# Optimization experiments

Hardware: AMD Instinct MI355X
Metric: run time of the kernel (lower is better)

## Reference

```python
import jax, jax.numpy as jnp
import numpy as np

HEADS = 16
DIM_HEAD = 64
INNER = HEADS * DIM_HEAD  # 1024
QUERY_DIM = 1024
CONTEXT_DIM = 1024
TEXT_LEN = 77
IMG_SCALE = 1.0
SCALE = DIM_HEAD ** -0.5


def setup_inputs() -> dict:
    key = jax.random.key(0)
    ks = jax.random.split(key, 10)
    B, N, Lc = 16, 2048, 333  # 77 text + 256 image tokens
    x = jax.random.normal(ks[0], (B, N, QUERY_DIM), dtype=jnp.float32)
    context = jax.random.normal(ks[1], (B, Lc, CONTEXT_DIM), dtype=jnp.float32)
    def w(k, din, dout):
        return jax.random.normal(k, (din, dout), dtype=jnp.float32) * (din ** -0.5)
    Wq = w(ks[2], QUERY_DIM, INNER)
    Wk = w(ks[3], CONTEXT_DIM, INNER)
    Wv = w(ks[4], CONTEXT_DIM, INNER)
    Wk_ip = w(ks[5], CONTEXT_DIM, INNER)
    Wv_ip = w(ks[6], CONTEXT_DIM, INNER)
    Wo = w(ks[7], INNER, QUERY_DIM)
    bo = jnp.zeros((QUERY_DIM,), dtype=jnp.float32)
    return {"x": x, "context": context, "Wq": Wq, "Wk": Wk, "Wv": Wv,
            "Wk_ip": Wk_ip, "Wv_ip": Wv_ip, "Wo": Wo, "bo": bo}


def _attend(q, k, v):
    # q: [B,N,H,D], k/v: [B,L,H,D]
    sim = jnp.einsum('bihd,bjhd->bhij', q, k) * SCALE
    attn = jax.nn.softmax(sim, axis=-1)
    out = jnp.einsum('bhij,bjhd->bihd', attn, v)
    B, N, H, D = out.shape
    return out.reshape(B, N, H * D)


def reference(x, context, Wq, Wk, Wv, Wk_ip, Wv_ip, Wo, bo):
    B, N, _ = x.shape
    ctx_txt = context[:, :TEXT_LEN, :]
    ctx_img = context[:, TEXT_LEN:, :]
    q = (x @ Wq).reshape(B, N, HEADS, DIM_HEAD)
    k = (ctx_txt @ Wk).reshape(B, TEXT_LEN, HEADS, DIM_HEAD)
    v = (ctx_txt @ Wv).reshape(B, TEXT_LEN, HEADS, DIM_HEAD)
    out = _attend(q, k, v)
    Li = ctx_img.shape[1]
    k_ip = (ctx_img @ Wk_ip).reshape(B, Li, HEADS, DIM_HEAD)
    v_ip = (ctx_img @ Wv_ip).reshape(B, Li, HEADS, DIM_HEAD)
    out_ip = _attend(q, k_ip, v_ip)
    out = out + IMG_SCALE * out_ip
    return out @ Wo + bo
```

## Files before the change

### kernel.cpp

```cpp
#include <hip/hip_runtime.h>
#include <cstdint>
#include <type_traits>

typedef unsigned short u16;
typedef __attribute__((ext_vector_type(8))) short short8;
typedef __attribute__((ext_vector_type(4))) float f32x4;

__device__ __forceinline__ u16 f2bf(float f) {
  unsigned x;
  __builtin_memcpy(&x, &f, 4);
  x = x + 0x7fffu + ((x >> 16) & 1u);
  return (u16)(x >> 16);
}
__device__ __forceinline__ f32x4 mfma16(short8 a, short8 b, f32x4 c) {
  return __builtin_amdgcn_mfma_f32_16x16x32_bf16(a, b, c, 0, 0, 0);
}
__device__ __forceinline__ void async_cp16(const u16* g, const u16* l) {
  __builtin_amdgcn_global_load_lds(
      (const __attribute__((address_space(1))) unsigned int*)(uintptr_t)g,
      (__attribute__((address_space(3))) unsigned int*)(uintptr_t)l, 16, 0, 0);
}

__global__ __launch_bounds__(256)
void cvt_f32_bf16(const float* __restrict__ s, u16* __restrict__ d, long n4) {
  long i = (long)blockIdx.x * 256 + threadIdx.x;
  if (i < n4) {
    float4 f = ((const float4*)s)[i];
    ushort4 o;
    o.x = f2bf(f.x);
    o.y = f2bf(f.y);
    o.z = f2bf(f.z);
    o.w = f2bf(f.w);
    ((ushort4*)d)[i] = o;
  }
}

__global__ __launch_bounds__(256)
void zero16(u16* __restrict__ p, long n8) {
  long i = (long)blockIdx.x * 256 + threadIdx.x;
  if (i < n8) {
    short8 z = {0, 0, 0, 0, 0, 0, 0, 0};
    ((short8*)p)[i] = z;
  }
}

struct TP { const float* s[6]; u16* d[6]; };

__global__ __launch_bounds__(256)
void transpose6(TP a) {
  __shared__ float tile[32][33];
  const float* S = a.s[blockIdx.z];
  u16* D = a.d[blockIdx.z];
  const int tx = threadIdx.x, ty = threadIdx.y;
  const int bx = blockIdx.x * 32, by = blockIdx.y * 32;
#pragma unroll
  for (int i = 0; i < 32; i += 8)
    tile[ty + i][tx] = S[(long)(by + ty + i) * 1024 + bx + tx];
  __syncthreads();
#pragma unroll
  for (int i = 0; i < 32; i += 8)
    D[(long)(bx + ty + i) * 1024 + by + tx] = f2bf(tile[tx][ty + i]);
}

template <typename CT, bool VT>
__global__ __launch_bounds__(256, 2)
void gemm_bt(const u16* __restrict__ A, const u16* __restrict__ Bt0,
             const u16* __restrict__ Bt1, CT* __restrict__ C0,
             CT* __restrict__ C1, const float* __restrict__ bias,
             int M, int RPB, int BSTR, int ROFF, int vtcol) {
  const u16* Bt = (blockIdx.z == 0) ? Bt0 : Bt1;
  CT* C = (blockIdx.z == 0) ? C0 : C1;
  __shared__ u16 As[128 * 32];
  __shared__ u16 Bs[128 * 32];
  const int t = threadIdx.x;
  const int w = t >> 6, lane = t & 63;
  const int m0 = blockIdx.x * 128, n0 = blockIdx.y * 128;
  const int subk = (lane & 3) * 8;

  long ag[2], bg[2];
  int lo[2];
#pragma unroll
  for (int r = 0; r < 2; ++r) {
    int m = m0 + r * 64 + w * 16 + (lane >> 2);
    if (m >= M) m = M - 1;
    long row = (long)(m / RPB) * BSTR + (m % RPB) + ROFF;
    ag[r] = row * 1024 + subk;
    lo[r] = r * 2048 + w * 512 + (lane >> 2) * 32 + subk;
    int n = n0 + r * 64 + w * 16 + (lane >> 2);
    bg[r] = (long)n * 1024 + subk;
  }
  const int wm = w >> 1, wn = w & 1;
  const int lr = lane & 15, quad = lane >> 4;
  const u16* Ap = As + (wm * 64 + lr) * 32 + quad * 8;
  const u16* Bp = Bs + (wn * 64 + lr) * 32 + quad * 8;

  const f32x4 fz = {0.f, 0.f, 0.f, 0.f};
  f32x4 acc[4][4];
#pragma unroll
  for (int i = 0; i < 4; ++i)
#pragma unroll
    for (int j = 0; j < 4; ++j) acc[i][j] = fz;

  for (int k0 = 0; k0 < 1024; k0 += 32) {
    __syncthreads();
    async_cp16(A + ag[0] + k0, As + lo[0]);
    async_cp16(A + ag[1] + k0, As + lo[1]);
    async_cp16(Bt + bg[0] + k0, Bs + lo[0]);
    async_cp16(Bt + bg[1] + k0, Bs + lo[1]);
    __syncthreads();
    short8 a[4], b[4];
#pragma unroll
    for (int i = 0; i < 4; ++i) a[i] = *(const short8*)(Ap + i * 512);
#pragma unroll
    for (int i = 0; i < 4; ++i) b[i] = *(const short8*)(Bp + i * 512);
#pragma unroll
    for (int i = 0; i < 4; ++i)
#pragma unroll
      for (int j = 0; j < 4; ++j) acc[i][j] = mfma16(a[i], b[j], acc[i][j]);
  }

  if constexpr (VT) {
    if (blockIdx.z == 1) {
#pragma unroll
      for (int i = 0; i < 4; ++i)
#pragma unroll
        for (int r = 0; r < 4; ++r) {
          int m = m0 + wm * 64 + i * 16 + quad * 4 + r;
          if (m < M) {
            long vrow = (long)(m / RPB) * 1024;
            int j = m % RPB;
#pragma unroll
            for (int jj = 0; jj < 4; ++jj) {
              int n = n0 + wn * 64 + jj * 16 + lr;
              C[(vrow + n) * 384 + vtcol + j] = (CT)f2bf(acc[i][jj][r]);
            }
          }
        }
      return;
    }
  }
#pragma unroll
  for (int i = 0; i < 4; ++i) {
#pragma unroll
    for (int r = 0; r < 4; ++r) {
      int m = m0 + wm * 64 + i * 16 + quad * 4 + r;
      if (m < M) {
        long crow = ((long)(m / RPB) * BSTR + (m % RPB) + ROFF) * 1024;
#pragma unroll
        for (int j = 0; j < 4; ++j) {
          int n = n0 + wn * 64 + j * 16 + lr;
          float v = acc[i][j][r];
          if (bias) v += bias[n];
          if constexpr (std::is_same<CT, float>::value)
            C[crow + n] = v;
          else
            C[crow + n] = f2bf(v);
        }
      }
    }
  }
}

__device__ __forceinline__ void stage_vt(const u16* __restrict__ vrow,
                                         int colbase, u16* Vt, int t) {
#pragma unroll
  for (int it = 0; it < 4; ++it) {
    int G = it * 256 + t;
    int r = G >> 4, p = G & 15;
    int g = p ^ (r & 7);
    async_cp16(vrow + (long)r * 384 + colbase + g * 8, Vt + G * 8);
  }
}

template <int JT>
__device__ __forceinline__ void qk_mm(const u16* __restrict__ kbase, short8 aq0,
                                      short8 aq1, int lr, int quad,
                                      f32x4* sacc) {
#pragma unroll
  for (int jt = 0; jt < JT; ++jt) {
    const u16* kp = kbase + (long)(jt * 16 + lr) * 1024 + quad * 8;
    short8 b0 = *(const short8*)kp;
    short8 b1 = *(const short8*)(kp + 32);
    f32x4 z = {0.f, 0.f, 0.f, 0.f};
    z = mfma16(aq0, b0, z);
    sacc[jt] = mfma16(aq1, b1, z);
  }
}

template <int JT>
__device__ __forceinline__ void pv_mm(const u16* Vt, const u16* Pb, int w,
                                      int lr, int quad, f32x4* oacc) {
#pragma unroll
  for (int c = 0; c < JT / 2; ++c) {
    short8 pf = *(const short8*)(Pb + (w * 16 + lr) * 136 + c * 32 + quad * 8);
#pragma unroll
    for (int nt = 0; nt < 4; ++nt) {
      int g = (c * 4 + quad) ^ (lr & 7);
      short8 vf = *(const short8*)(Vt + (nt * 16 + lr) * 128 + g * 8);
      oacc[nt] = mfma16(pf, vf, oacc[nt]);
    }
  }
}

__device__ __forceinline__ void img_chunk(int koff, int colbase,
                                          const u16* __restrict__ kbh,
                                          const u16* __restrict__ vbh, u16* Vt,
                                          u16* Pb, short8 aq0, short8 aq1,
                                          f32x4 (&oi)[4], float (&mrun)[4],
                                          float (&lrun)[4], int t, int w,
                                          int lr, int quad) {
  __syncthreads();
  stage_vt(vbh, colbase, Vt, t);
  f32x4 sacc[8];
  qk_mm<8>(kbh + (long)koff * 1024, aq0, aq1, lr, quad, sacc);
#pragma unroll
  for (int r = 0; r < 4; ++r) {
    float mprev = mrun[r];
    float mx = mprev;
#pragma unroll
    for (int jt = 0; jt < 8; ++jt) {
      float v = sacc[jt][r] * 0.125f;
      sacc[jt][r] = v;
      mx = fmaxf(mx, v);
    }
#pragma unroll
    for (int d = 1; d < 16; d <<= 1) mx = fmaxf(mx, __shfl_xor(mx, d, 64));
    float sc = __expf(mprev - mx);
    int row = w * 16 + quad * 4 + r;
    float s = 0.f;
#pragma unroll
    for (int jt = 0; jt < 8; ++jt) {
      float p = __expf(sacc[jt][r] - mx);
      s += p;
      Pb[row * 136 + jt * 16 + lr] = f2bf(p);
    }
#pragma unroll
    for (int d = 1; d < 16; d <<= 1) s += __shfl_xor(s, d, 64);
    lrun[r] = lrun[r] * sc + s;
    mrun[r] = mx;
#pragma unroll
    for (int nt = 0; nt < 4; ++nt) oi[nt][r] *= sc;
  }
  __syncthreads();
  pv_mm<8>(Vt, Pb, w, lr, quad, oi);
}

__global__ __launch_bounds__(256, 4)
void attn_kernel(u16* __restrict__ q, const u16* __restrict__ kall,
                 const u16* __restrict__ vtg) {
  __shared__ u16 Vt[64 * 128];
  __shared__ u16 Pb[64 * 136];
  const int t = threadIdx.x;
  const int w = t >> 6, lane = t & 63;
  const int lr = lane & 15, quad = lane >> 4;
  const int bq = blockIdx.x, h = blockIdx.y, b = blockIdx.z;
  const long qrow = (long)(b * 2048 + bq * 64 + w * 16 + lr) * 1024 + h * 64;
  short8 aq0 = *(const short8*)(q + qrow + quad * 8);
  short8 aq1 = *(const short8*)(q + qrow + 32 + quad * 8);
  const f32x4 fz = {0.f, 0.f, 0.f, 0.f};
  f32x4 ot[4], oi[4];
#pragma unroll
  for (int i = 0; i < 4; ++i) { ot[i] = fz; oi[i] = fz; }
  float mrun[4], lrun[4];
#pragma unroll
  for (int r = 0; r < 4; ++r) { mrun[r] = -3.0e38f; lrun[r] = 0.f; }
  const u16* kbh = kall + (long)b * 333 * 1024 + h * 64;
  const u16* vbh = vtg + (long)(b * 16 + h) * 64 * 384;

  stage_vt(vbh, 0, Vt, t);
  {
    f32x4 sacc[6];
    qk_mm<6>(kbh, aq0, aq1, lr, quad, sacc);
#pragma unroll
    for (int r = 0; r < 4; ++r) {
      float mx = -3.0e38f;
#pragma unroll
      for (int jt = 0; jt < 6; ++jt) {
        int j = jt * 16 + lr;
        float v = (j < 77) ? sacc[jt][r] * 0.125f : -3.0e38f;
        sacc[jt][r] = v;
        mx = fmaxf(mx, v);
      }
#pragma unroll
      for (int d = 1; d < 16; d <<= 1) mx = fmaxf(mx, __shfl_xor(mx, d, 64));
      float s = 0.f;
#pragma unroll
      for (int jt = 0; jt < 6; ++jt) {
        float p = __expf(sacc[jt][r] - mx);
        sacc[jt][r] = p;
        s += p;
      }
#pragma unroll
      for (int d = 1; d < 16; d <<= 1) s += __shfl_xor(s, d, 64);
      float is = 1.0f / s;
      int row = w * 16 + quad * 4 + r;
#pragma unroll
      for (int jt = 0; jt < 6; ++jt)
        Pb[row * 136 + jt * 16 + lr] = f2bf(sacc[jt][r] * is);
    }
    __syncthreads();
    pv_mm<6>(Vt, Pb, w, lr, quad, ot);
  }
  img_chunk(77, 96, kbh, vbh, Vt, Pb, aq0, aq1, oi, mrun, lrun, t, w, lr, quad);
  img_chunk(205, 224, kbh, vbh, Vt, Pb, aq0, aq1, oi, mrun, lrun, t, w, lr, quad);

#pragma unroll
  for (int r = 0; r < 4; ++r) {
    float il = 1.0f / lrun[r];
    long row = (long)(b * 2048 + bq * 64 + w * 16 + quad * 4 + r);
#pragma unroll
    for (int nt = 0; nt < 4; ++nt)
      q[row * 1024 + h * 64 + nt * 16 + lr] = f2bf(ot[nt][r] + oi[nt][r] * il);
  }
}

extern "C" void kernel_launch(void* const* d_in, const int* in_sizes, int n_in,
                              void* d_out, int out_size, void* d_ws,
                              size_t ws_size, hipStream_t stream) {
  const float* x = (const float*)d_in[0];
  const float* ctx = (const float*)d_in[1];
  u16* ws = (u16*)d_ws;
  u16* WT[6];
  for (int i = 0; i < 6; ++i) WT[i] = ws + (size_t)i * (1u << 20);
  u16* xb = ws + (size_t)6 * (1u << 20);
  u16* qb = xb + (size_t)(1u << 25);
  u16* ctxb = qb + (size_t)(1u << 25);
  u16* kall = ctxb + (size_t)16 * 333 * 1024;
  u16* vtg = xb;
  float* out = (float*)d_out;

  cvt_f32_bf16<<<dim3(32768), dim3(256), 0, stream>>>(x, xb, 8388608);
  cvt_f32_bf16<<<dim3(5328), dim3(256), 0, stream>>>(ctx, ctxb, 1363968);

  TP tp;
  tp.s[0] = (const float*)d_in[2]; tp.d[0] = WT[0];
  tp.s[1] = (const float*)d_in[3]; tp.d[1] = WT[1];
  tp.s[2] = (const float*)d_in[4]; tp.d[2] = WT[2];
  tp.s[3] = (const float*)d_in[5]; tp.d[3] = WT[3];
  tp.s[4] = (const float*)d_in[6]; tp.d[4] = WT[4];
  tp.s[5] = (const float*)d_in[7]; tp.d[5] = WT[5];
  transpose6<<<dim3(32, 32, 6), dim3(32, 8, 1), 0, stream>>>(tp);

  gemm_bt<u16, false><<<dim3(256, 8, 1), dim3(256), 0, stream>>>(
      xb, WT[0], WT[0], qb, qb, (const float*)nullptr, 32768, 2048, 2048, 0, -1);
  zero16<<<dim3(3072), dim3(256), 0, stream>>>(vtg, 786432);
  gemm_bt<u16, true><<<dim3(10, 8, 2), dim3(256), 0, stream>>>(
      ctxb, WT[1], WT[2], kall, vtg, (const float*)nullptr, 1232, 77, 333, 0, 0);
  gemm_bt<u16, true><<<dim3(32, 8, 2), dim3(256), 0, stream>>>(
      ctxb, WT[3], WT[4], kall, vtg, (const float*)nullptr, 4096, 256, 333, 77, 96);
  attn_kernel<<<dim3(32, 16, 16), dim3(256), 0, stream>>>(qb, kall, vtg);
  gemm_bt<float, false><<<dim3(256, 8, 1), dim3(256), 0, stream>>>(
      qb, WT[5], WT[5], out, out, (const float*)d_in[8], 32768, 2048, 2048, 0, -1);
}
```

Before: 704.8 us.

## Read V straight from global in attention, drop LDS staging and barriers

Removes the async V staging into shared memory and the block-wide barriers around it; the PV MFMA now loads V fragments directly from global/L2. The P buffer stays in LDS, but each wave reads back only its own rows. Softmax switches to exp2 with a prescaled log2e constant, the text-branch normalization is deferred to the epilogue, and the occupancy hint rises from 4 to 5 blocks per CU. The cost is that every wave fetches the whole V tile from L2, roughly four times the V traffic, with less coalesced accesses.

```diff
diff --git a/kernel.cpp b/kernel.cpp
--- a/kernel.cpp
+++ b/kernel.cpp
@@ -19,6 +19,9 @@
   __builtin_amdgcn_global_load_lds(
       (const __attribute__((address_space(1))) unsigned int*)(uintptr_t)g,
       (__attribute__((address_space(3))) unsigned int*)(uintptr_t)l, 16, 0, 0);
+}
+__device__ __forceinline__ float fexp2(float x) {
+  return __builtin_amdgcn_exp2f(x);
 }
 
 __global__ __launch_bounds__(256)
@@ -161,17 +164,6 @@
   }
 }
 
-__device__ __forceinline__ void stage_vt(const u16* __restrict__ vrow,
-                                         int colbase, u16* Vt, int t) {
-#pragma unroll
-  for (int it = 0; it < 4; ++it) {
-    int G = it * 256 + t;
-    int r = G >> 4, p = G & 15;
-    int g = p ^ (r & 7);
-    async_cp16(vrow + (long)r * 384 + colbase + g * 8, Vt + G * 8);
-  }
-}
-
 template <int JT>
 __device__ __forceinline__ void qk_mm(const u16* __restrict__ kbase, short8 aq0,
                                       short8 aq1, int lr, int quad,
@@ -188,29 +180,30 @@
 }
 
 template <int JT>
-__device__ __forceinline__ void pv_mm(const u16* Vt, const u16* Pb, int w,
-                                      int lr, int quad, f32x4* oacc) {
+__device__ __forceinline__ void pv_mm(const u16* __restrict__ Vg,
+                                      const u16* Pb, int w, int lr, int quad,
+                                      f32x4* oacc) {
 #pragma unroll
   for (int c = 0; c < JT / 2; ++c) {
     short8 pf = *(const short8*)(Pb + (w * 16 + lr) * 136 + c * 32 + quad * 8);
 #pragma unroll
     for (int nt = 0; nt < 4; ++nt) {
-      int g = (c * 4 + quad) ^ (lr & 7);
-      short8 vf = *(const short8*)(Vt + (nt * 16 + lr) * 128 + g * 8);
+      short8 vf =
+          *(const short8*)(Vg + (long)(nt * 16 + lr) * 384 + c * 32 + quad * 8);
       oacc[nt] = mfma16(pf, vf, oacc[nt]);
     }
   }
 }
+
+#define SCL2 0.18033688011112042f
 
 __device__ __forceinline__ void img_chunk(int koff, int colbase,
                                           const u16* __restrict__ kbh,
-                                          const u16* __restrict__ vbh, u16* Vt,
-                                          u16* Pb, short8 aq0, short8 aq1,
+                                          const u16* __restrict__ vbh, u16* Pb,
+                                          short8 aq0, short8 aq1,
                                           f32x4 (&oi)[4], float (&mrun)[4],
-                                          float (&lrun)[4], int t, int w,
-                                          int lr, int quad) {
-  __syncthreads();
-  stage_vt(vbh, colbase, Vt, t);
+                                          float (&lrun)[4], int w, int lr,
+                                          int quad) {
   f32x4 sacc[8];
   qk_mm<8>(kbh + (long)koff * 1024, aq0, aq1, lr, quad, sacc);
 #pragma unroll
@@ -219,18 +212,18 @@
     float mx = mprev;
 #pragma unroll
     for (int jt = 0; jt < 8; ++jt) {
-      float v = sacc[jt][r] * 0.125f;
+      float v = sacc[jt][r] * SCL2;
       sacc[jt][r] = v;
       mx = fmaxf(mx, v);
     }
 #pragma unroll
     for (int d = 1; d < 16; d <<= 1) mx = fmaxf(mx, __shfl_xor(mx, d, 64));
-    float sc = __expf(mprev - mx);
+    float sc = fexp2(mprev - mx);
     int row = w * 16 + quad * 4 + r;
     float s = 0.f;
 #pragma unroll
     for (int jt = 0; jt < 8; ++jt) {
-      float p = __expf(sacc[jt][r] - mx);
+      float p = fexp2(sacc[jt][r] - mx);
       s += p;
       Pb[row * 136 + jt * 16 + lr] = f2bf(p);
     }
@@ -241,14 +234,12 @@
 #pragma unroll
     for (int nt = 0; nt < 4; ++nt) oi[nt][r] *= sc;
   }
-  __syncthreads();
-  pv_mm<8>(Vt, Pb, w, lr, quad, oi);
-}
-
-__global__ __launch_bounds__(256, 4)
+  pv_mm<8>(vbh + colbase, Pb, w, lr, quad, oi);
+}
+
+__global__ __launch_bounds__(256, 5)
 void attn_kernel(u16* __restrict__ q, const u16* __restrict__ kall,
                  const u16* __restrict__ vtg) {
-  __shared__ u16 Vt[64 * 128];
   __shared__ u16 Pb[64 * 136];
   const int t = threadIdx.x;
   const int w = t >> 6, lane = t & 63;
@@ -261,13 +252,12 @@
   f32x4 ot[4], oi[4];
 #pragma unroll
   for (int i = 0; i < 4; ++i) { ot[i] = fz; oi[i] = fz; }
-  float mrun[4], lrun[4];
+  float mrun[4], lrun[4], st[4];
 #pragma unroll
   for (int r = 0; r < 4; ++r) { mrun[r] = -3.0e38f; lrun[r] = 0.f; }
   const u16* kbh = kall + (long)b * 333 * 1024 + h * 64;
   const u16* vbh = vtg + (long)(b * 16 + h) * 64 * 384;
 
-  stage_vt(vbh, 0, Vt, t);
   {
     f32x4 sacc[6];
     qk_mm<6>(kbh, aq0, aq1, lr, quad, sacc);
@@ -277,40 +267,38 @@
 #pragma unroll
       for (int jt = 0; jt < 6; ++jt) {
         int j = jt * 16 + lr;
-        float v = (j < 77) ? sacc[jt][r] * 0.125f : -3.0e38f;
+        float v = (j < 77) ? sacc[jt][r] * SCL2 : -3.0e38f;
         sacc[jt][r] = v;
         mx = fmaxf(mx, v);
       }
 #pragma unroll
       for (int d = 1; d < 16; d <<= 1) mx = fmaxf(mx, __shfl_xor(mx, d, 64));
       float s = 0.f;
+      int row = w * 16 + quad * 4 + r;
 #pragma unroll
       for (int jt = 0; jt < 6; ++jt) {
-        float p = __expf(sacc[jt][r] - mx);
-        sacc[jt][r] = p;
+        float p = fexp2(sacc[jt][r] - mx);
         s += p;
+        Pb[row * 136 + jt * 16 + lr] = f2bf(p);
       }
 #pragma unroll
       for (int d = 1; d < 16; d <<= 1) s += __shfl_xor(s, d, 64);
-      float is = 1.0f / s;
-      int row = w * 16 + quad * 4 + r;
-#pragma unroll
-      for (int jt = 0; jt < 6; ++jt)
-        Pb[row * 136 + jt * 16 + lr] = f2bf(sacc[jt][r] * is);
-    }
-    __syncthreads();
-    pv_mm<6>(Vt, Pb, w, lr, quad, ot);
-  }
-  img_chunk(77, 96, kbh, vbh, Vt, Pb, aq0, aq1, oi, mrun, lrun, t, w, lr, quad);
-  img_chunk(205, 224, kbh, vbh, Vt, Pb, aq0, aq1, oi, mrun, lrun, t, w, lr, quad);
+      st[r] = s;
+    }
+    pv_mm<6>(vbh, Pb, w, lr, quad, ot);
+  }
+  img_chunk(77, 96, kbh, vbh, Pb, aq0, aq1, oi, mrun, lrun, w, lr, quad);
+  img_chunk(205, 224, kbh, vbh, Pb, aq0, aq1, oi, mrun, lrun, w, lr, quad);
 
 #pragma unroll
   for (int r = 0; r < 4; ++r) {
+    float ist = 1.0f / st[r];
     float il = 1.0f / lrun[r];
     long row = (long)(b * 2048 + bq * 64 + w * 16 + quad * 4 + r);
 #pragma unroll
     for (int nt = 0; nt < 4; ++nt)
-      q[row * 1024 + h * 64 + nt * 16 + lr] = f2bf(ot[nt][r] + oi[nt][r] * il);
+      q[row * 1024 + h * 64 + nt * 16 + lr] =
+          f2bf(ot[nt][r] * ist + oi[nt][r] * il);
   }
 }
 
```

Measured after the change: 837.6 us. 18.9% more time.
